# Optimization experiments

Measured on AMD Instinct MI355X. Metric: run time of the kernel, lower is better.

## Reference

```python
import jax, jax.numpy as jnp
import numpy as np

N = 10000
E = 320000
D_IN = 256
D_H = 256
D_OUT = 64
NEG_SLOPE = 0.2


def _segment_softmax(scores, seg, num_segments):
    # numerically stable softmax over variable-size neighborhoods
    m = jax.ops.segment_max(scores, seg, num_segments=num_segments)
    e = jnp.exp(scores - m[seg])
    s = jax.ops.segment_sum(e, seg, num_segments=num_segments)
    return e / s[seg]


def _gatv2_conv(x, src, dst, Wl, bl, Wr, br, att, bias):
    # PyG GATv2Conv, heads=1: lin_l on source, lin_r on target
    xl = x @ Wl + bl              # [N, C]
    xr = x @ Wr + br              # [N, C]
    xj = xl[src]                  # [E, C] source messages
    e = jax.nn.leaky_relu(xj + xr[dst], NEG_SLOPE)   # [E, C]
    score = e @ att               # [E]
    alpha = _segment_softmax(score, dst, N)          # [E]
    out = jax.ops.segment_sum(alpha[:, None] * xj, dst, num_segments=N)
    return out + bias


def setup_inputs() -> dict:
    key = jax.random.key(0)
    ks = jax.random.split(key, 16)
    s1 = 1.0 / np.sqrt(D_IN)
    s2 = 1.0 / np.sqrt(D_H)
    x = jax.random.normal(ks[0], (N, D_IN), dtype=jnp.float32)
    edge_index = jax.random.randint(ks[1], (2, E), 0, N, dtype=jnp.int64)
    return {
        "x": x,
        "W1l": jax.random.normal(ks[2], (D_IN, D_H), jnp.float32) * s1,
        "b1l": jnp.zeros((D_H,), jnp.float32),
        "W1r": jax.random.normal(ks[3], (D_IN, D_H), jnp.float32) * s1,
        "b1r": jnp.zeros((D_H,), jnp.float32),
        "att1": jax.random.normal(ks[4], (D_H,), jnp.float32) * s2,
        "bias1": jnp.zeros((D_H,), jnp.float32),
        "W2l": jax.random.normal(ks[5], (D_H, D_H), jnp.float32) * s2,
        "b2l": jnp.zeros((D_H,), jnp.float32),
        "W2r": jax.random.normal(ks[6], (D_H, D_H), jnp.float32) * s2,
        "b2r": jnp.zeros((D_H,), jnp.float32),
        "att2": jax.random.normal(ks[7], (D_H,), jnp.float32) * s2,
        "bias2": jnp.zeros((D_H,), jnp.float32),
        "Wout": jax.random.normal(ks[8], (D_H, D_OUT), jnp.float32) * s2,
        "bout": jnp.zeros((D_OUT,), jnp.float32),
        "edge_index": edge_index,
    }


def reference(x, W1l, b1l, W1r, b1r, att1, bias1,
              W2l, b2l, W2r, b2r, att2, bias2,
              Wout, bout, edge_index):
    # add self loops (PyG GATv2Conv default)
    loops = jnp.arange(N, dtype=edge_index.dtype)
    src = jnp.concatenate([edge_index[0], loops])
    dst = jnp.concatenate([edge_index[1], loops])

    h = _gatv2_conv(x, src, dst, W1l, b1l, W1r, b1r, att1, bias1)
    h = jax.nn.relu(h)            # norm=Identity, dropout inactive (eval)
    h = _gatv2_conv(h, src, dst, W2l, b2l, W2r, b2r, att2, bias2)
    h = jax.nn.relu(h)
    logits = h @ Wout + bout      # [N, D_OUT]
    return jax.nn.log_softmax(logits, axis=1)
```

## Files before the change

kernel.cpp:

```cpp
#include <hip/hip_runtime.h>
#include <hip/hip_bf16.h>
#include <math.h>

#define N_NODES 10000
#define N_EDGES 320000
#define TOT_E (N_EDGES + N_NODES)
#define D 256
#define DOUT 64
#define NEG_SLOPE 0.2f
#define MAXDEG 128

typedef __attribute__((ext_vector_type(8))) short bf16x8;
typedef __attribute__((ext_vector_type(4))) float f32x4;
typedef unsigned short ushort_t;

__device__ __forceinline__ unsigned short f2b_rne(float f) {
    unsigned int x = __float_as_uint(f);
    x += 0x7FFFu + ((x >> 16) & 1u);
    return (unsigned short)(x >> 16);
}
__device__ __forceinline__ float b2f(unsigned short h) {
    return __uint_as_float(((unsigned int)h) << 16);
}
__device__ __forceinline__ void bsplit(float v, unsigned short& hi, unsigned short& lo) {
    hi = f2b_rne(v);
    lo = f2b_rne(v - b2f(hi));
}

__device__ __forceinline__ void gload16(const ushort_t* g, ushort_t* l) {
    __builtin_amdgcn_global_load_lds(
        (const __attribute__((address_space(1))) void*)g,
        (__attribute__((address_space(3))) void*)l, 16, 0, 0);
}

__device__ __forceinline__ bool detect_f32(const void* x) {
    const ushort_t* xb = (const ushort_t*)x;
    int lane = threadIdx.x & 63;
    int bad = 0;
    #pragma unroll
    for (int i = 0; i < 4; ++i) {
        float v = b2f(xb[2 * (lane + 64 * i)]);
        bad += !(fabsf(v) < 1e4f) ? 1 : 0;
    }
    #pragma unroll
    for (int o = 32; o > 0; o >>= 1) bad += __shfl_down(bad, o);
    return __shfl(bad, 0) > 8;
}
__device__ __forceinline__ bool detect_i64(const int* e32) {
    int lane = threadIdx.x & 63;
    int nz = (e32[2 * lane + 1] != 0) ? 1 : 0;
    #pragma unroll
    for (int o = 32; o > 0; o >>= 1) nz += __shfl_down(nz, o);
    return __shfl(nz, 0) == 0;
}

__global__ __launch_bounds__(256) void prep_kernel(
        const void* x, ushort_t* xh, ushort_t* xlo,
        const void* W1l, const void* W1r, const void* W2l, const void* W2r, const void* Wo,
        const void* v0, const void* v1, const void* v2, const void* v3,
        const void* v4, const void* v5, const void* v6, const void* v7, const void* v8,
        ushort_t* wt, float* vecf, int* counts) {
    bool f32s = detect_f32(x);
    int bid = blockIdx.x;
    int t = threadIdx.x;
    if (bid < 2500) {
        int i = bid * 1024 + t * 4;
        float v[4];
        if (f32s) {
            float4 f = *(const float4*)((const float*)x + i);
            v[0] = f.x; v[1] = f.y; v[2] = f.z; v[3] = f.w;
        } else {
            union { uint2 q; ushort_t u[4]; } r;
            r.q = *(const uint2*)((const ushort_t*)x + i);
            #pragma unroll
            for (int j = 0; j < 4; ++j) v[j] = b2f(r.u[j]);
        }
        union { uint2 q; ushort_t u[4]; } H, L;
        #pragma unroll
        for (int j = 0; j < 4; ++j) bsplit(v[j], H.u[j], L.u[j]);
        *(uint2*)(xh + i) = H.q;
        *(uint2*)(xlo + i) = L.q;
    } else if (bid < 3588) {
        int b = bid - 2500;
        const void* srcs5[5] = {W1l, W1r, W2l, W2r, Wo};
        int wid, n, ncols;
        if (b < 1024) { wid = b >> 8; n = b & 255; ncols = 256; }
        else          { wid = 4;      n = b - 1024; ncols = 64; }
        ushort_t* dh;
        ushort_t* dl;
        if (wid < 4) { dh = wt + (size_t)wid * 2 * 65536; dl = dh + 65536; }
        else         { dh = wt + (size_t)8 * 65536;       dl = dh + 16384; }
        float v = f32s ? ((const float*)srcs5[wid])[(size_t)t * ncols + n]
                       : b2f(((const ushort_t*)srcs5[wid])[(size_t)t * ncols + n]);
        unsigned short hi, lo;
        bsplit(v, hi, lo);
        dh[(size_t)n * 256 + t] = hi;
        dl[(size_t)n * 256 + t] = lo;
    } else if (bid < 3597) {
        int b = bid - 3588;
        const void* ps[9] = {v0, v1, v2, v3, v4, v5, v6, v7, v8};
        int n = (b == 8) ? DOUT : 256;
        if (t < n) {
            float v = f32s ? ((const float*)ps[b])[t] : b2f(((const ushort_t*)ps[b])[t]);
            vecf[b * 256 + t] = v;
        }
    } else {
        int idx = (bid - 3597) * 256 + t;
        if (idx < N_NODES) counts[idx] = 0;
    }
}

__device__ __forceinline__ int eload(const int* ei, bool is64, int idx) {
    int v = is64 ? ei[2 * (size_t)idx] : ei[idx];
    return ((unsigned)v < (unsigned)N_NODES) ? v : 0;
}

__global__ __launch_bounds__(256) void scatter_kernel(const int* __restrict__ ei,
                                                      int* __restrict__ counts,
                                                      int* __restrict__ srcs_pad) {
    bool is64 = detect_i64(ei);
    int id = blockIdx.x * 256 + threadIdx.x;
    if (id >= TOT_E) return;
    int src, dst;
    if (id < N_EDGES) { src = eload(ei, is64, id); dst = eload(ei, is64, N_EDGES + id); }
    else              { src = dst = id - N_EDGES; }
    int slot = atomicAdd(&counts[dst], 1);
    if (slot < MAXDEG) srcs_pad[dst * MAXDEG + slot] = src;
}

__global__ __launch_bounds__(256, 3) void gemm_mfma_kernel(
        const ushort_t* __restrict__ Ahg, const ushort_t* __restrict__ Alg,
        const ushort_t* __restrict__ Wh0, const ushort_t* __restrict__ Wl0,
        const float* __restrict__ bias0, ushort_t* __restrict__ out0,
        const ushort_t* __restrict__ Wh1, const ushort_t* __restrict__ Wl1,
        const float* __restrict__ bias1, float* __restrict__ out1) {
    __shared__ __align__(16) ushort_t AhL[2][4096];
    __shared__ __align__(16) ushort_t AlL[2][4096];
    __shared__ __align__(16) ushort_t BhL[2][2048];
    __shared__ __align__(16) ushort_t BlL[2][2048];
    int tid = threadIdx.x;
    int lane = tid & 63, wave = tid >> 6;
    int lin = blockIdx.x + 8 * blockIdx.y;
    int v = (lin & 7) * 79 + (lin >> 3);
    int row0 = (v >> 3) * 128;
    int y = v & 7;
    const ushort_t* Wh; const ushort_t* Wl; const float* bias;
    int col0;
    bool ob_bf16;
    if (y < 4) { Wh = Wh0; Wl = Wl0; bias = bias0; col0 = y * 64; ob_bf16 = true; }
    else       { Wh = Wh1; Wl = Wl1; bias = bias1; col0 = (y - 4) * 64; ob_bf16 = false; }

    const ushort_t* gp[6];
    ushort_t* lp0[6];
    ushort_t* lp1[6];
    {
        int lane4 = lane >> 2;
        int qsl = (lane & 3) ^ (lane4 & 3);
        #pragma unroll
        for (int j = 0; j < 6; ++j) {
            int q = wave * 6 + j;
            if (q < 8) {
                gp[j] = Ahg + (size_t)(row0 + q * 16 + lane4) * 256 + qsl * 8;
                lp0[j] = &AhL[0][q * 512]; lp1[j] = &AhL[1][q * 512];
            } else if (q < 16) {
                int r = q - 8;
                gp[j] = Alg + (size_t)(row0 + r * 16 + lane4) * 256 + qsl * 8;
                lp0[j] = &AlL[0][r * 512]; lp1[j] = &AlL[1][r * 512];
            } else if (q < 20) {
                int r = q - 16;
                gp[j] = Wh + (size_t)(col0 + r * 16 + lane4) * 256 + qsl * 8;
                lp0[j] = &BhL[0][r * 512]; lp1[j] = &BhL[1][r * 512];
            } else {
                int r = q - 20;
                gp[j] = Wl + (size_t)(col0 + r * 16 + lane4) * 256 + qsl * 8;
                lp0[j] = &BlL[0][r * 512]; lp1[j] = &BlL[1][r * 512];
            }
        }
    }
    int wm = wave >> 1, wn = wave & 1;
    int l15 = lane & 15;
    int slot = (lane >> 4) ^ (lane & 3);

    f32x4 acc[4][2];
    #pragma unroll
    for (int mg = 0; mg < 4; ++mg)
        #pragma unroll
        for (int ng = 0; ng < 2; ++ng) acc[mg][ng] = (f32x4){0.f, 0.f, 0.f, 0.f};

    #pragma unroll
    for (int j = 0; j < 6; ++j) { gload16(gp[j], lp0[j]); gp[j] += 32; }
    __syncthreads();

    #pragma unroll
    for (int s = 0; s < 8; ++s) {
        const int cb = s & 1;
        if (s < 7) {
            #pragma unroll
            for (int j = 0; j < 6; ++j) {
                gload16(gp[j], cb ? lp0[j] : lp1[j]);
                gp[j] += 32;
            }
        }
        bf16x8 ah[4], al[4];
        #pragma unroll
        for (int mg = 0; mg < 4; ++mg) {
            int o = (wm * 64 + mg * 16 + l15) * 32 + slot * 8;
            ah[mg] = *(const bf16x8*)&AhL[cb][o];
            al[mg] = *(const bf16x8*)&AlL[cb][o];
        }
        #pragma unroll
        for (int ng = 0; ng < 2; ++ng) {
            int o = (wn * 32 + ng * 16 + l15) * 32 + slot * 8;
            bf16x8 b_h = *(const bf16x8*)&BhL[cb][o];
            bf16x8 b_l = *(const bf16x8*)&BlL[cb][o];
            #pragma unroll
            for (int mg = 0; mg < 4; ++mg) {
                acc[mg][ng] = __builtin_amdgcn_mfma_f32_16x16x32_bf16(ah[mg], b_l, acc[mg][ng], 0, 0, 0);
                acc[mg][ng] = __builtin_amdgcn_mfma_f32_16x16x32_bf16(al[mg], b_h, acc[mg][ng], 0, 0, 0);
                acc[mg][ng] = __builtin_amdgcn_mfma_f32_16x16x32_bf16(ah[mg], b_h, acc[mg][ng], 0, 0, 0);
            }
        }
        __syncthreads();
    }

    int quad = lane >> 4;
    #pragma unroll
    for (int ng = 0; ng < 2; ++ng) {
        int col = col0 + wn * 32 + ng * 16 + l15;
        float bv = bias[col];
        #pragma unroll
        for (int mg = 0; mg < 4; ++mg) {
            #pragma unroll
            for (int i = 0; i < 4; ++i) {
                int row = row0 + wm * 64 + mg * 16 + quad * 4 + i;
                if (row < N_NODES) {
                    float vv = acc[mg][ng][i] + bv;
                    if (ob_bf16) out0[(size_t)row * D + col] = f2b_rne(vv);
                    else         out1[(size_t)row * D + col] = vv;
                }
            }
        }
    }
}

__global__ __launch_bounds__(256) void conv_kernel(const ushort_t* __restrict__ xl,
                                                   const float* __restrict__ xr,
                                                   const float* __restrict__ att,
                                                   const float* __restrict__ bias,
                                                   const int* __restrict__ counts,
                                                   const int* __restrict__ srcs_pad,
                                                   ushort_t* __restrict__ hh,
                                                   ushort_t* __restrict__ hl) {
    __shared__ float xr_s[D];
    __shared__ int srcs_s[MAXDEG];
    __shared__ float hwmax[2][8];
    __shared__ float sred[8];
    __shared__ float fbuf[8][256];
    int node = blockIdx.x;
    int t = threadIdx.x;
    int deg = counts[node];
    if (deg > MAXDEG) deg = MAXDEG;
    if (deg <= 0) {
        float o = fmaxf(bias[t], 0.f);
        unsigned short hi, lo; bsplit(o, hi, lo);
        hh[(size_t)node * D + t] = hi;
        hl[(size_t)node * D + t] = lo;
        return;
    }
    xr_s[t] = xr[(size_t)node * D + t];
    if (t < deg) srcs_s[t] = srcs_pad[node * MAXDEG + t];
    __syncthreads();

    int hw = t >> 5;
    int seg = t & 31;
    float xr8[8], att8[8];
    {
        float4 x0 = *(const float4*)&xr_s[seg * 8];
        float4 x1 = *(const float4*)&xr_s[seg * 8 + 4];
        float4 a0 = *(const float4*)(att + seg * 8);
        float4 a1 = *(const float4*)(att + seg * 8 + 4);
        xr8[0] = x0.x; xr8[1] = x0.y; xr8[2] = x0.z; xr8[3] = x0.w;
        xr8[4] = x1.x; xr8[5] = x1.y; xr8[6] = x1.z; xr8[7] = x1.w;
        att8[0] = a0.x; att8[1] = a0.y; att8[2] = a0.z; att8[3] = a0.w;
        att8[4] = a1.x; att8[5] = a1.y; att8[6] = a1.z; att8[7] = a1.w;
    }
    float acc8[8];
    #pragma unroll
    for (int j = 0; j < 8; ++j) acc8[j] = 0.f;
    float m = -INFINITY, s = 0.f;
    int par = 0;

    for (int cbase = 0; cbase < deg; cbase += 32, par ^= 1) {
        int dlim = deg - cbase; if (dlim > 32) dlim = 32;
        int ni = (dlim > hw) ? ((dlim - hw + 7) >> 3) : 0;
        union { uint4 q; ushort_t u[8]; } r[4];
        float scv[4];
        #pragma unroll
        for (int i = 0; i < 4; ++i) {
            if (i < ni) {
                int src = srcs_s[cbase + hw + 8 * i];
                r[i].q = *(const uint4*)(xl + (size_t)src * D + seg * 8);
            }
        }
        #pragma unroll
        for (int i = 0; i < 4; ++i) {
            scv[i] = -1e30f;
            if (i < ni) {
                float p = 0.f;
                #pragma unroll
                for (int j = 0; j < 8; ++j) {
                    float v = b2f(r[i].u[j]) + xr8[j];
                    v = fmaxf(v, NEG_SLOPE * v);
                    p = fmaf(v, att8[j], p);
                }
                #pragma unroll
                for (int o = 16; o > 0; o >>= 1) p += __shfl_xor(p, o, 32);
                scv[i] = isfinite(p) ? p : -1e30f;
            }
        }
        float mx4 = fmaxf(fmaxf(scv[0], scv[1]), fmaxf(scv[2], scv[3]));
        if (seg == 0) hwmax[par][hw] = mx4;
        __syncthreads();
        float cmax = hwmax[par][0];
        #pragma unroll
        for (int k = 1; k < 8; ++k) cmax = fmaxf(cmax, hwmax[par][k]);
        float m_new = fmaxf(m, cmax);
        float scale = (m > -1e37f) ? __expf(m - m_new) : 0.f;
        s *= scale;
        #pragma unroll
        for (int j = 0; j < 8; ++j) acc8[j] *= scale;
        #pragma unroll
        for (int i = 0; i < 4; ++i) {
            if (i < ni) {
                float p = __expf(scv[i] - m_new);
                s += p;
                #pragma unroll
                for (int j = 0; j < 8; ++j) {
                    acc8[j] = fmaf(p, b2f(r[i].u[j]), acc8[j]);
                }
            }
        }
        m = m_new;
    }
    __syncthreads();
    float4 w0 = (float4){acc8[0], acc8[1], acc8[2], acc8[3]};
    float4 w1 = (float4){acc8[4], acc8[5], acc8[6], acc8[7]};
    *(float4*)&fbuf[hw][seg * 8] = w0;
    *(float4*)&fbuf[hw][seg * 8 + 4] = w1;
    if (seg == 0) sred[hw] = s;
    __syncthreads();
    float tot = 0.f;
    #pragma unroll
    for (int k = 0; k < 8; ++k) tot += fbuf[k][t];
    float stot = sred[0];
    #pragma unroll
    for (int k = 1; k < 8; ++k) stot += sred[k];
    float o = tot / stot + bias[t];
    if (!isfinite(o)) o = 0.f;
    o = fmaxf(o, 0.f);
    unsigned short hi, lo; bsplit(o, hi, lo);
    hh[(size_t)node * D + t] = hi;
    hl[(size_t)node * D + t] = lo;
}

__global__ __launch_bounds__(256) void logits_kernel(
        const ushort_t* __restrict__ Ahg, const ushort_t* __restrict__ Alg,
        const ushort_t* __restrict__ Wh, const ushort_t* __restrict__ Wl,
        const float* __restrict__ bias, float* __restrict__ out) {
    __shared__ bf16x8 Ah[4][64];
    __shared__ bf16x8 Al[4][64];
    __shared__ bf16x8 Bh[4][64];
    __shared__ bf16x8 Bl[4][64];
    __shared__ float Cs[64][65];
    __shared__ float mxs[64], lss[64];
    int tid = threadIdx.x;
    int lane = tid & 63, wave = tid >> 6;
    int row0 = blockIdx.x * 64;
    int sm = tid >> 2, skq = tid & 3;
    int sl = skq * 16 + (sm & 15), sr = sm >> 4;

    f32x4 acc[4];
    #pragma unroll
    for (int c = 0; c < 4; ++c) acc[c] = (f32x4){0.f, 0.f, 0.f, 0.f};

    for (int k0 = 0; k0 < D; k0 += 32) {
        uint4 qah, qal;
        int grow = row0 + sm;
        if (grow < N_NODES) {
            size_t aoff = (size_t)grow * D + k0 + skq * 8;
            qah = *(const uint4*)(Ahg + aoff);
            qal = *(const uint4*)(Alg + aoff);
        } else {
            qah = (uint4){0, 0, 0, 0}; qal = (uint4){0, 0, 0, 0};
        }
        size_t boff = (size_t)sm * 256 + k0 + skq * 8;
        uint4 qbh = *(const uint4*)(Wh + boff);
        uint4 qbl = *(const uint4*)(Wl + boff);
        __syncthreads();
        *(uint4*)&Ah[sr][sl] = qah;
        *(uint4*)&Al[sr][sl] = qal;
        *(uint4*)&Bh[sr][sl] = qbh;
        *(uint4*)&Bl[sr][sl] = qbl;
        __syncthreads();
        bf16x8 a_h = Ah[wave][lane];
        bf16x8 a_l = Al[wave][lane];
        #pragma unroll
        for (int c = 0; c < 4; ++c) {
            bf16x8 b_h = Bh[c][lane];
            bf16x8 b_l = Bl[c][lane];
            acc[c] = __builtin_amdgcn_mfma_f32_16x16x32_bf16(a_h, b_l, acc[c], 0, 0, 0);
            acc[c] = __builtin_amdgcn_mfma_f32_16x16x32_bf16(a_l, b_h, acc[c], 0, 0, 0);
            acc[c] = __builtin_amdgcn_mfma_f32_16x16x32_bf16(a_h, b_h, acc[c], 0, 0, 0);
        }
    }
    int quad = lane >> 4;
    #pragma unroll
    for (int c = 0; c < 4; ++c) {
        int col = c * 16 + (lane & 15);
        float bv = bias[col];
        #pragma unroll
        for (int i = 0; i < 4; ++i) {
            int row = wave * 16 + quad * 4 + i;
            Cs[row][col] = acc[c][i] + bv;
        }
    }
    __syncthreads();
    if (tid < 64) {
        float mx = -INFINITY;
        for (int c2 = 0; c2 < 64; ++c2) {
            float v = Cs[tid][c2];
            if (!isfinite(v)) { v = -1e30f; Cs[tid][c2] = v; }
            mx = fmaxf(mx, v);
        }
        float ssum = 0.f;
        for (int c2 = 0; c2 < 64; ++c2) ssum += expf(Cs[tid][c2] - mx);
        mxs[tid] = mx;
        lss[tid] = logf(ssum);
    }
    __syncthreads();
    for (int idx = tid; idx < 64 * 64; idx += 256) {
        int r = idx >> 6, col = idx & 63;
        int grow = row0 + r;
        if (grow < N_NODES) out[(size_t)grow * DOUT + col] = Cs[r][col] - mxs[r] - lss[r];
    }
}

extern "C" void kernel_launch(void* const* d_in, const int* in_sizes, int n_in,
                              void* d_out, int out_size, void* d_ws, size_t ws_size,
                              hipStream_t stream) {
    const void* x    = d_in[0];
    const void* W1l  = d_in[1];
    const void* b1l  = d_in[2];
    const void* W1r  = d_in[3];
    const void* b1r  = d_in[4];
    const void* att1 = d_in[5];
    const void* bia1 = d_in[6];
    const void* W2l  = d_in[7];
    const void* b2l  = d_in[8];
    const void* W2r  = d_in[9];
    const void* b2r  = d_in[10];
    const void* att2 = d_in[11];
    const void* bia2 = d_in[12];
    const void* Wout = d_in[13];
    const void* bout = d_in[14];
    const int*  ei   = (const int*)d_in[15];

    int* counts   = (int*)d_ws;
    int* srcs_pad = counts + N_NODES;
    ushort_t* wt = (ushort_t*)(srcs_pad + (size_t)N_NODES * MAXDEG);
    ushort_t* W1lH = wt;                ushort_t* W1lL = W1lH + 65536;
    ushort_t* W1rH = W1lL + 65536;      ushort_t* W1rL = W1rH + 65536;
    ushort_t* W2lH = W1rL + 65536;      ushort_t* W2lL = W2lH + 65536;
    ushort_t* W2rH = W2lL + 65536;      ushort_t* W2rL = W2rH + 65536;
    ushort_t* WoH  = W2rL + 65536;      ushort_t* WoL  = WoH + 16384;
    float* vecf = (float*)(WoL + 16384);
    ushort_t* xh  = (ushort_t*)(vecf + 9 * 256);
    ushort_t* xlo = xh + (size_t)N_NODES * D;
    ushort_t* xlb = xlo + (size_t)N_NODES * D;
    float* xr = (float*)(xlb + (size_t)N_NODES * D);
    ushort_t* hh = xh;
    ushort_t* hl = xlo;

    float* b1lf = vecf + 0 * 256;
    float* b1rf = vecf + 1 * 256;
    float* att1f = vecf + 2 * 256;
    float* bia1f = vecf + 3 * 256;
    float* b2lf = vecf + 4 * 256;
    float* b2rf = vecf + 5 * 256;
    float* att2f = vecf + 6 * 256;
    float* bia2f = vecf + 7 * 256;
    float* boutf = vecf + 8 * 256;

    prep_kernel<<<3637, 256, 0, stream>>>(x, xh, xlo,
                                          W1l, W1r, W2l, W2r, Wout,
                                          b1l, b1r, att1, bia1, b2l, b2r, att2, bia2, bout,
                                          wt, vecf, counts);
    scatter_kernel<<<(TOT_E + 255) / 256, 256, 0, stream>>>(ei, counts, srcs_pad);

    gemm_mfma_kernel<<<dim3(8, 79), 256, 0, stream>>>(
        xh, xlo, W1lH, W1lL, b1lf, xlb, W1rH, W1rL, b1rf, xr);
    conv_kernel<<<N_NODES, 256, 0, stream>>>(xlb, xr, att1f, bia1f, counts, srcs_pad, hh, hl);
    gemm_mfma_kernel<<<dim3(8, 79), 256, 0, stream>>>(
        hh, hl, W2lH, W2lL, b2lf, xlb, W2rH, W2rL, b2rf, xr);
    conv_kernel<<<N_NODES, 256, 0, stream>>>(xlb, xr, att2f, bia2f, counts, srcs_pad, hh, hl);
    logits_kernel<<<(N_NODES + 63) / 64, 256, 0, stream>>>(hh, hl, WoH, WoL, boutf, (float*)d_out);
}
```

Baseline: 265.1 us.

## Map one wavefront per node in GATv2 aggregation, drop shared-memory syncs

The conv kernel now assigns one 64-lane wavefront per destination node, with four nodes per block, instead of a whole 256-thread block per node. Each lane owns four channels and walks edges four at a time. Source indices are broadcast with shuffles and the online softmax runs entirely in registers, so the per-chunk __syncthreads and the final cross-wave LDS reduction are gone. In exchange there is less memory-level parallelism per node, since only four edge rows are in flight per wave, and each score needs a 64-lane shuffle reduction.

```diff
diff --git a/kernel.cpp b/kernel.cpp
--- a/kernel.cpp
+++ b/kernel.cpp
@@ -251,116 +251,95 @@
                                                    const int* __restrict__ srcs_pad,
                                                    ushort_t* __restrict__ hh,
                                                    ushort_t* __restrict__ hl) {
-    __shared__ float xr_s[D];
-    __shared__ int srcs_s[MAXDEG];
-    __shared__ float hwmax[2][8];
-    __shared__ float sred[8];
-    __shared__ float fbuf[8][256];
-    int node = blockIdx.x;
-    int t = threadIdx.x;
+    int lane = threadIdx.x & 63;
+    int node = blockIdx.x * 4 + (threadIdx.x >> 6);
+    if (node >= N_NODES) return;
+    int c0 = lane * 4;
+    float4 bi4 = *(const float4*)(bias + c0);
     int deg = counts[node];
     if (deg > MAXDEG) deg = MAXDEG;
     if (deg <= 0) {
-        float o = fmaxf(bias[t], 0.f);
-        unsigned short hi, lo; bsplit(o, hi, lo);
-        hh[(size_t)node * D + t] = hi;
-        hl[(size_t)node * D + t] = lo;
+        union { uint2 q; ushort_t u[4]; } H, L;
+        #pragma unroll
+        for (int j = 0; j < 4; ++j) {
+            float o = fmaxf(((const float*)&bi4)[j], 0.f);
+            bsplit(o, H.u[j], L.u[j]);
+        }
+        *(uint2*)(hh + (size_t)node * D + c0) = H.q;
+        *(uint2*)(hl + (size_t)node * D + c0) = L.q;
         return;
     }
-    xr_s[t] = xr[(size_t)node * D + t];
-    if (t < deg) srcs_s[t] = srcs_pad[node * MAXDEG + t];
-    __syncthreads();
-
-    int hw = t >> 5;
-    int seg = t & 31;
-    float xr8[8], att8[8];
-    {
-        float4 x0 = *(const float4*)&xr_s[seg * 8];
-        float4 x1 = *(const float4*)&xr_s[seg * 8 + 4];
-        float4 a0 = *(const float4*)(att + seg * 8);
-        float4 a1 = *(const float4*)(att + seg * 8 + 4);
-        xr8[0] = x0.x; xr8[1] = x0.y; xr8[2] = x0.z; xr8[3] = x0.w;
-        xr8[4] = x1.x; xr8[5] = x1.y; xr8[6] = x1.z; xr8[7] = x1.w;
-        att8[0] = a0.x; att8[1] = a0.y; att8[2] = a0.z; att8[3] = a0.w;
-        att8[4] = a1.x; att8[5] = a1.y; att8[6] = a1.z; att8[7] = a1.w;
-    }
-    float acc8[8];
-    #pragma unroll
-    for (int j = 0; j < 8; ++j) acc8[j] = 0.f;
+    float4 xr4 = *(const float4*)(xr + (size_t)node * D + c0);
+    float4 at4 = *(const float4*)(att + c0);
+    int s0 = srcs_pad[node * MAXDEG + lane];
+    int s1 = srcs_pad[node * MAXDEG + 64 + lane];
+
     float m = -INFINITY, s = 0.f;
-    int par = 0;
-
-    for (int cbase = 0; cbase < deg; cbase += 32, par ^= 1) {
-        int dlim = deg - cbase; if (dlim > 32) dlim = 32;
-        int ni = (dlim > hw) ? ((dlim - hw + 7) >> 3) : 0;
-        union { uint4 q; ushort_t u[8]; } r[4];
-        float scv[4];
+    float a0 = 0.f, a1 = 0.f, a2 = 0.f, a3 = 0.f;
+
+    for (int e0 = 0; e0 < deg; e0 += 4) {
+        int ne = deg - e0; if (ne > 4) ne = 4;
+        union { uint2 q; ushort_t u[4]; } r[4];
+        float p[4];
         #pragma unroll
         for (int i = 0; i < 4; ++i) {
-            if (i < ni) {
-                int src = srcs_s[cbase + hw + 8 * i];
-                r[i].q = *(const uint4*)(xl + (size_t)src * D + seg * 8);
+            if (i < ne) {
+                int e = e0 + i;
+                int src = __shfl((e < 64) ? s0 : s1, e & 63);
+                r[i].q = *(const uint2*)(xl + (size_t)src * D + c0);
             }
         }
         #pragma unroll
         for (int i = 0; i < 4; ++i) {
-            scv[i] = -1e30f;
-            if (i < ni) {
-                float p = 0.f;
+            p[i] = -1e30f;
+            if (i < ne) {
+                float pp = 0.f;
                 #pragma unroll
-                for (int j = 0; j < 8; ++j) {
-                    float v = b2f(r[i].u[j]) + xr8[j];
+                for (int j = 0; j < 4; ++j) {
+                    float v = b2f(r[i].u[j]) + ((const float*)&xr4)[j];
                     v = fmaxf(v, NEG_SLOPE * v);
-                    p = fmaf(v, att8[j], p);
+                    pp = fmaf(v, ((const float*)&at4)[j], pp);
                 }
                 #pragma unroll
-                for (int o = 16; o > 0; o >>= 1) p += __shfl_xor(p, o, 32);
-                scv[i] = isfinite(p) ? p : -1e30f;
-            }
-        }
-        float mx4 = fmaxf(fmaxf(scv[0], scv[1]), fmaxf(scv[2], scv[3]));
-        if (seg == 0) hwmax[par][hw] = mx4;
-        __syncthreads();
-        float cmax = hwmax[par][0];
-        #pragma unroll
-        for (int k = 1; k < 8; ++k) cmax = fmaxf(cmax, hwmax[par][k]);
-        float m_new = fmaxf(m, cmax);
-        float scale = (m > -1e37f) ? __expf(m - m_new) : 0.f;
-        s *= scale;
-        #pragma unroll
-        for (int j = 0; j < 8; ++j) acc8[j] *= scale;
+                for (int o = 32; o > 0; o >>= 1) pp += __shfl_xor(pp, o);
+                p[i] = isfinite(pp) ? pp : -1e30f;
+            }
+        }
+        float mx = fmaxf(fmaxf(p[0], p[1]), fmaxf(p[2], p[3]));
+        float m_new = fmaxf(m, mx);
+        float sc = __expf(m - m_new);
+        float w[4];
+        float ws = 0.f;
         #pragma unroll
         for (int i = 0; i < 4; ++i) {
-            if (i < ni) {
-                float p = __expf(scv[i] - m_new);
-                s += p;
-                #pragma unroll
-                for (int j = 0; j < 8; ++j) {
-                    acc8[j] = fmaf(p, b2f(r[i].u[j]), acc8[j]);
-                }
+            w[i] = (i < ne) ? __expf(p[i] - m_new) : 0.f;
+            ws += w[i];
+        }
+        s = s * sc + ws;
+        a0 *= sc; a1 *= sc; a2 *= sc; a3 *= sc;
+        #pragma unroll
+        for (int i = 0; i < 4; ++i) {
+            if (i < ne) {
+                a0 = fmaf(w[i], b2f(r[i].u[0]), a0);
+                a1 = fmaf(w[i], b2f(r[i].u[1]), a1);
+                a2 = fmaf(w[i], b2f(r[i].u[2]), a2);
+                a3 = fmaf(w[i], b2f(r[i].u[3]), a3);
             }
         }
         m = m_new;
     }
-    __syncthreads();
-    float4 w0 = (float4){acc8[0], acc8[1], acc8[2], acc8[3]};
-    float4 w1 = (float4){acc8[4], acc8[5], acc8[6], acc8[7]};
-    *(float4*)&fbuf[hw][seg * 8] = w0;
-    *(float4*)&fbuf[hw][seg * 8 + 4] = w1;
-    if (seg == 0) sred[hw] = s;
-    __syncthreads();
-    float tot = 0.f;
-    #pragma unroll
-    for (int k = 0; k < 8; ++k) tot += fbuf[k][t];
-    float stot = sred[0];
-    #pragma unroll
-    for (int k = 1; k < 8; ++k) stot += sred[k];
-    float o = tot / stot + bias[t];
-    if (!isfinite(o)) o = 0.f;
-    o = fmaxf(o, 0.f);
-    unsigned short hi, lo; bsplit(o, hi, lo);
-    hh[(size_t)node * D + t] = hi;
-    hl[(size_t)node * D + t] = lo;
+    float inv = 1.f / s;
+    float ov[4] = {a0 * inv, a1 * inv, a2 * inv, a3 * inv};
+    union { uint2 q; ushort_t u[4]; } H, L;
+    #pragma unroll
+    for (int j = 0; j < 4; ++j) {
+        float o = ov[j] + ((const float*)&bi4)[j];
+        if (!isfinite(o)) o = 0.f;
+        o = fmaxf(o, 0.f);
+        bsplit(o, H.u[j], L.u[j]);
+    }
+    *(uint2*)(hh + (size_t)node * D + c0) = H.q;
+    *(uint2*)(hl + (size_t)node * D + c0) = L.q;
 }
 
 __global__ __launch_bounds__(256) void logits_kernel(
@@ -499,9 +478,9 @@
 
     gemm_mfma_kernel<<<dim3(8, 79), 256, 0, stream>>>(
         xh, xlo, W1lH, W1lL, b1lf, xlb, W1rH, W1rL, b1rf, xr);
-    conv_kernel<<<N_NODES, 256, 0, stream>>>(xlb, xr, att1f, bia1f, counts, srcs_pad, hh, hl);
+    conv_kernel<<<(N_NODES + 3) / 4, 256, 0, stream>>>(xlb, xr, att1f, bia1f, counts, srcs_pad, hh, hl);
     gemm_mfma_kernel<<<dim3(8, 79), 256, 0, stream>>>(
         hh, hl, W2lH, W2lL, b2lf, xlb, W2rH, W2rL, b2rf, xr);
-    conv_kernel<<<N_NODES, 256, 0, stream>>>(xlb, xr, att2f, bia2f, counts, srcs_pad, hh, hl);
+    conv_kernel<<<(N_NODES + 3) / 4, 256, 0, stream>>>(xlb, xr, att2f, bia2f, counts, srcs_pad, hh, hl);
     logits_kernel<<<(N_NODES + 63) / 64, 256, 0, stream>>>(hh, hl, WoH, WoL, boutf, (float*)d_out);
 }
```

After: 291.7 us. +10.0%, slower.

## Quantize source messages to int8 and store xr as bf16 for conv gathers

Applied to the files above, without the earlier changes.

The GEMM now writes the target projection xr as bf16 instead of fp32. A new quant kernel converts the bf16 source projection xl to per-row int8 with one scale per row. The conv kernel gathers the 8-bit rows plus their scales, dequantizes them in registers, and uses the result for both attention scores and aggregation, which halves the bytes of the random neighbor gather. In exchange there is an extra kernel launch and pass over xl, plus the precision loss of int8 quantization, which may push results past tolerance.

```diff
diff --git a/kernel.cpp b/kernel.cpp
--- a/kernel.cpp
+++ b/kernel.cpp
@@ -133,7 +133,7 @@
         const ushort_t* __restrict__ Wh0, const ushort_t* __restrict__ Wl0,
         const float* __restrict__ bias0, ushort_t* __restrict__ out0,
         const ushort_t* __restrict__ Wh1, const ushort_t* __restrict__ Wl1,
-        const float* __restrict__ bias1, float* __restrict__ out1) {
+        const float* __restrict__ bias1, ushort_t* __restrict__ out1) {
     __shared__ __align__(16) ushort_t AhL[2][4096];
     __shared__ __align__(16) ushort_t AlL[2][4096];
     __shared__ __align__(16) ushort_t BhL[2][2048];
@@ -145,10 +145,10 @@
     int row0 = (v >> 3) * 128;
     int y = v & 7;
     const ushort_t* Wh; const ushort_t* Wl; const float* bias;
+    ushort_t* outp;
     int col0;
-    bool ob_bf16;
-    if (y < 4) { Wh = Wh0; Wl = Wl0; bias = bias0; col0 = y * 64; ob_bf16 = true; }
-    else       { Wh = Wh1; Wl = Wl1; bias = bias1; col0 = (y - 4) * 64; ob_bf16 = false; }
+    if (y < 4) { Wh = Wh0; Wl = Wl0; bias = bias0; col0 = y * 64; outp = out0; }
+    else       { Wh = Wh1; Wl = Wl1; bias = bias1; col0 = (y - 4) * 64; outp = out1; }
 
     const ushort_t* gp[6];
     ushort_t* lp0[6];
@@ -235,16 +235,45 @@
                 int row = row0 + wm * 64 + mg * 16 + quad * 4 + i;
                 if (row < N_NODES) {
                     float vv = acc[mg][ng][i] + bv;
-                    if (ob_bf16) out0[(size_t)row * D + col] = f2b_rne(vv);
-                    else         out1[(size_t)row * D + col] = vv;
+                    outp[(size_t)row * D + col] = f2b_rne(vv);
                 }
             }
         }
     }
 }
 
-__global__ __launch_bounds__(256) void conv_kernel(const ushort_t* __restrict__ xl,
-                                                   const float* __restrict__ xr,
+__global__ __launch_bounds__(256) void quant_kernel(const ushort_t* __restrict__ xin,
+                                                    unsigned char* __restrict__ xq,
+                                                    float* __restrict__ xscale) {
+    int lane = threadIdx.x & 63;
+    int row = blockIdx.x * 4 + (threadIdx.x >> 6);
+    if (row >= N_NODES) return;
+    union { uint2 q; ushort_t u[4]; } r;
+    r.q = *(const uint2*)(xin + (size_t)row * D + lane * 4);
+    float v[4];
+    float am = 0.f;
+    #pragma unroll
+    for (int j = 0; j < 4; ++j) {
+        v[j] = b2f(r.u[j]);
+        if (!isfinite(v[j])) v[j] = 0.f;
+        am = fmaxf(am, fabsf(v[j]));
+    }
+    #pragma unroll
+    for (int o = 32; o > 0; o >>= 1) am = fmaxf(am, __shfl_xor(am, o));
+    float inv = (am > 0.f) ? 127.f / am : 0.f;
+    unsigned int pk = 0;
+    #pragma unroll
+    for (int j = 0; j < 4; ++j) {
+        int qv = (int)rintf(v[j] * inv);
+        pk |= ((unsigned int)(qv & 255)) << (8 * j);
+    }
+    *(unsigned int*)(xq + (size_t)row * D + lane * 4) = pk;
+    if (lane == 0) xscale[row] = (am > 0.f) ? am / 127.f : 0.f;
+}
+
+__global__ __launch_bounds__(256) void conv_kernel(const unsigned char* __restrict__ xq,
+                                                   const float* __restrict__ xscale,
+                                                   const ushort_t* __restrict__ xrb,
                                                    const float* __restrict__ att,
                                                    const float* __restrict__ bias,
                                                    const int* __restrict__ counts,
@@ -253,6 +282,7 @@
                                                    ushort_t* __restrict__ hl) {
     __shared__ float xr_s[D];
     __shared__ int srcs_s[MAXDEG];
+    __shared__ float sscale_s[MAXDEG];
     __shared__ float hwmax[2][8];
     __shared__ float sred[8];
     __shared__ float fbuf[8][256];
@@ -267,8 +297,12 @@
         hl[(size_t)node * D + t] = lo;
         return;
     }
-    xr_s[t] = xr[(size_t)node * D + t];
-    if (t < deg) srcs_s[t] = srcs_pad[node * MAXDEG + t];
+    xr_s[t] = b2f(xrb[(size_t)node * D + t]);
+    if (t < deg) {
+        int s = srcs_pad[node * MAXDEG + t];
+        srcs_s[t] = s;
+        sscale_s[t] = xscale[s];
+    }
     __syncthreads();
 
     int hw = t >> 5;
@@ -293,23 +327,31 @@
     for (int cbase = 0; cbase < deg; cbase += 32, par ^= 1) {
         int dlim = deg - cbase; if (dlim > 32) dlim = 32;
         int ni = (dlim > hw) ? ((dlim - hw + 7) >> 3) : 0;
-        union { uint4 q; ushort_t u[8]; } r[4];
+        uint2 r[4];
+        float xf[4][8];
         float scv[4];
         #pragma unroll
         for (int i = 0; i < 4; ++i) {
             if (i < ni) {
                 int src = srcs_s[cbase + hw + 8 * i];
-                r[i].q = *(const uint4*)(xl + (size_t)src * D + seg * 8);
+                r[i] = *(const uint2*)(xq + (size_t)src * D + seg * 8);
             }
         }
         #pragma unroll
         for (int i = 0; i < 4; ++i) {
             scv[i] = -1e30f;
             if (i < ni) {
+                float se = sscale_s[cbase + hw + 8 * i];
+                #pragma unroll
+                for (int j = 0; j < 8; ++j) {
+                    unsigned int w32 = (j < 4) ? r[i].x : r[i].y;
+                    int iv = ((int)(w32 << (24 - 8 * (j & 3)))) >> 24;
+                    xf[i][j] = (float)iv * se;
+                }
                 float p = 0.f;
                 #pragma unroll
                 for (int j = 0; j < 8; ++j) {
-                    float v = b2f(r[i].u[j]) + xr8[j];
+                    float v = xf[i][j] + xr8[j];
                     v = fmaxf(v, NEG_SLOPE * v);
                     p = fmaf(v, att8[j], p);
                 }
@@ -336,7 +378,7 @@
                 s += p;
                 #pragma unroll
                 for (int j = 0; j < 8; ++j) {
-                    acc8[j] = fmaf(p, b2f(r[i].u[j]), acc8[j]);
+                    acc8[j] = fmaf(p, xf[i][j], acc8[j]);
                 }
             }
         }
@@ -477,7 +519,9 @@
     ushort_t* xh  = (ushort_t*)(vecf + 9 * 256);
     ushort_t* xlo = xh + (size_t)N_NODES * D;
     ushort_t* xlb = xlo + (size_t)N_NODES * D;
-    float* xr = (float*)(xlb + (size_t)N_NODES * D);
+    ushort_t* xrb = xlb + (size_t)N_NODES * D;
+    unsigned char* xq = (unsigned char*)(xrb + (size_t)N_NODES * D);
+    float* xscale = (float*)(xq + (size_t)N_NODES * D);
     ushort_t* hh = xh;
     ushort_t* hl = xlo;
 
@@ -498,10 +542,14 @@
     scatter_kernel<<<(TOT_E + 255) / 256, 256, 0, stream>>>(ei, counts, srcs_pad);
 
     gemm_mfma_kernel<<<dim3(8, 79), 256, 0, stream>>>(
-        xh, xlo, W1lH, W1lL, b1lf, xlb, W1rH, W1rL, b1rf, xr);
-    conv_kernel<<<N_NODES, 256, 0, stream>>>(xlb, xr, att1f, bia1f, counts, srcs_pad, hh, hl);
+        xh, xlo, W1lH, W1lL, b1lf, xlb, W1rH, W1rL, b1rf, xrb);
+    quant_kernel<<<(N_NODES + 3) / 4, 256, 0, stream>>>(xlb, xq, xscale);
+    conv_kernel<<<N_NODES, 256, 0, stream>>>(xq, xscale, xrb, att1f, bia1f,
+                                             counts, srcs_pad, hh, hl);
     gemm_mfma_kernel<<<dim3(8, 79), 256, 0, stream>>>(
-        hh, hl, W2lH, W2lL, b2lf, xlb, W2rH, W2rL, b2rf, xr);
-    conv_kernel<<<N_NODES, 256, 0, stream>>>(xlb, xr, att2f, bia2f, counts, srcs_pad, hh, hl);
+        hh, hl, W2lH, W2lL, b2lf, xlb, W2rH, W2rL, b2rf, xrb);
+    quant_kernel<<<(N_NODES + 3) / 4, 256, 0, stream>>>(xlb, xq, xscale);
+    conv_kernel<<<N_NODES, 256, 0, stream>>>(xq, xscale, xrb, att2f, bia2f,
+                                             counts, srcs_pad, hh, hl);
     logits_kernel<<<(N_NODES + 63) / 64, 256, 0, stream>>>(hh, hl, WoH, WoL, boutf, (float*)d_out);
 }
```

New measurement: 265.4 us. Within noise of the previous version (+0.1%).
